# Kernel tuning notes

Hardware: AMD Instinct MI355X
Metric: run time of the kernel (lower is better)

## Reference

```python
import jax, jax.numpy as jnp
import numpy as np

K = 16          # self.nn_size
BALL2 = 0.2     # ball_size * 2, compared against squared L2 dists (faiss convention)

def _knn(q, db, k):
    # squared L2 pairwise distances (B,N,M) via ||q||^2 + ||db||^2 - 2 q.db
    d2 = (jnp.sum(q * q, -1)[..., None]
          + jnp.sum(db * db, -1)[..., None, :]
          - 2.0 * jnp.einsum('bnc,bmc->bnm', q, db))
    neg_d, idx = jax.lax.top_k(-d2, k)   # k smallest distances
    return -neg_d, idx                    # (B,N,K), (B,N,K)

def _cond_numbers(grouped, nball, B, N, C):
    # center by masked-ball mean, then singular values of (K,C) groups
    center = jnp.sum(grouped, axis=2, keepdims=True) / nball[..., None]
    centered = (grouped - center).reshape(-1, K, C)
    S = jnp.linalg.svd(centered, compute_uv=False)   # descending, (B*N, min(K,C))
    return (S[:, 0] / (S[:, -1] + S[:, 0])).reshape(B, N)

def setup_inputs() -> dict:
    key = jax.random.key(0)
    k1, k2 = jax.random.split(key)
    ref_points = jax.random.uniform(k1, (2, 8192, 3), dtype=jnp.float32)
    points = jax.random.uniform(k2, (2, 8192, 3), dtype=jnp.float32)
    return {"ref_points": ref_points, "points": points}

def reference(ref_points, points):
    B, N, C = ref_points.shape
    dist, idx = _knn(ref_points, ref_points, K)
    mask = dist < BALL2                                  # (B,N,K)
    nball = jnp.sum(mask.astype(ref_points.dtype), -1, keepdims=True)  # (B,N,1)

    gather = jax.vmap(lambda p, i: p[i])                 # (N,C),(N,K)->(N,K,C)
    grouped_ref = gather(ref_points, idx)                # (B,N,K,C)
    grouped_ref = jnp.where(mask[..., None], grouped_ref, 0.0)  # masked_fill_ (in-place, kept)
    ref_cond = _cond_numbers(grouped_ref, nball, B, N, C)

    grouped = gather(points, idx)                        # (B,N,K,C)
    # NOTE: original calls masked_fill (non-inplace) and DISCARDS the result -> no masking here
    cond = _cond_numbers(grouped, nball, B, N, C)

    # metric: MSE with mean reduction
    return jnp.mean((cond - ref_cond) ** 2)
```

## Files before the change

### kernel.cpp

```cpp
#include <hip/hip_runtime.h>

#define NPTS   8192
#define KNN    16
#define G      10
#define NCELLS 1000
#define CELLSZ 0.1f
#define BALL2f 0.2f
#define TRUNCM 0xFFFFE000u
#define IDXM   0x1FFFu
#define NBLK   256
#define FLTMAX 3.402823466e+38f

#define WS_ACC    0
#define WS_DONE   8
#define WS_STARTS 16
#define WS_RSORT  8032

__device__ __forceinline__ int clampg(int v) { return v < 0 ? 0 : (v > G - 1 ? G - 1 : v); }

__global__ __launch_bounds__(1024) void prep_kernel(
        const float* __restrict__ ref, int* __restrict__ gstarts,
        float4* __restrict__ rs, double* __restrict__ acc, int* __restrict__ done) {
    __shared__ int cnt[NCELLS];
    __shared__ int ssum[NCELLS + 1];
    __shared__ int wsum[16];
    const int b = blockIdx.x, t = threadIdx.x;
    const int w = t >> 6, lane = t & 63;
    if (b == 0 && t == 0) { acc[0] = 0.0; done[0] = 0; }
    if (t < NCELLS) cnt[t] = 0;
    __syncthreads();

    const float4* rb4 = reinterpret_cast<const float4*>(ref + (size_t)b * NPTS * 3) + t * 6;
    float4 A = rb4[0], B = rb4[1], C = rb4[2], D = rb4[3], E = rb4[4], F = rb4[5];
    float xs[8] = {A.x, A.w, B.z, C.y, D.x, D.w, E.z, F.y};
    float ys[8] = {A.y, B.x, B.w, C.z, D.y, E.x, E.w, F.z};
    float zs[8] = {A.z, B.y, C.x, C.w, D.z, E.y, F.x, F.w};
    int cells[8], slots[8];
    #pragma unroll
    for (int k = 0; k < 8; ++k) {
        int c = (clampg((int)(zs[k] * (float)G)) * G + clampg((int)(ys[k] * (float)G))) * G
              + clampg((int)(xs[k] * (float)G));
        cells[k] = c;
        slots[k] = atomicAdd(&cnt[c], 1);
    }
    __syncthreads();

    int v = (t < NCELLS) ? cnt[t] : 0;
    #pragma unroll
    for (int off = 1; off < 64; off <<= 1) {
        int u = __shfl_up(v, off, 64);
        if (lane >= off) v += u;
    }
    if (lane == 63) wsum[w] = v;
    __syncthreads();
    if (t == 0) {
        int run = 0;
        for (int i2 = 0; i2 < 16; ++i2) { int tv = wsum[i2]; wsum[i2] = run; run += tv; }
    }
    __syncthreads();
    if (t < NCELLS) ssum[t + 1] = v + wsum[w];
    if (t == 0) ssum[0] = 0;
    __syncthreads();
    if (t <= NCELLS) gstarts[b * (NCELLS + 1) + t] = ssum[t];

    #pragma unroll
    for (int k = 0; k < 8; ++k) {
        int pos = ssum[cells[k]] + slots[k];
        rs[(size_t)b * NPTS + pos] = make_float4(xs[k], ys[k], zs[k],
                                                 __uint_as_float((unsigned)(t * 8 + k)));
    }
}

__device__ __noinline__ double cond3(double xx, double xy, double xz,
                                     double yy, double yz, double zz) {
    double q  = (xx + yy + zz) * (1.0 / 3.0);
    double a  = xx - q, b = yy - q, c = zz - q;
    double p1 = xy * xy + xz * xz + yz * yz;
    double p2 = a * a + b * b + c * c + 2.0 * p1;
    if (p2 <= 0.0) return 0.5;
    double p   = sqrt(p2 * (1.0 / 6.0));
    double inv = 1.0 / p;
    double b00 = a * inv, b11 = b * inv, b22 = c * inv;
    double b01 = xy * inv, b02 = xz * inv, b12 = yz * inv;
    double detB = b00 * (b11 * b22 - b12 * b12)
                - b01 * (b01 * b22 - b12 * b02)
                + b02 * (b01 * b12 - b11 * b02);
    double r = 0.5 * detB;
    r = fmin(1.0, fmax(-1.0, r));
    double phi = acos(r) * (1.0 / 3.0);
    double l0 = q + 2.0 * p * cos(phi);
    double l2 = q + 2.0 * p * cos(phi + 2.0943951023931953);
    double s0 = sqrt(fmax(l0, 0.0));
    double s2 = sqrt(fmax(l2, 0.0));
    return s0 / (s0 + s2);
}

__global__ __launch_bounds__(256) void cond_knn_kernel(
        const float* __restrict__ ref, const float* __restrict__ pts,
        const float4* __restrict__ rs, const int* __restrict__ gstarts,
        double* __restrict__ acc, int* __restrict__ done,
        float* __restrict__ out) {
    __shared__ float4 sdb[NPTS];
    __shared__ int ss[NCELLS + 1];
    __shared__ unsigned sld[2][64][17];
    __shared__ unsigned cutp[64];
    __shared__ unsigned char doneA[64];
    __shared__ int flagS;

    const int tid  = threadIdx.x;
    const int w    = tid >> 6;
    const int lane = tid & 63;
    const int b     = blockIdx.x >> 7;
    const int qbase = (blockIdx.x & 127) << 6;
    const float4* rs4 = rs + (size_t)b * NPTS;

    for (int i = tid; i < NPTS; i += 256) sdb[i] = rs4[i];
    for (int i = tid; i < NCELLS + 1; i += 256) ss[i] = gstarts[b * (NCELLS + 1) + i];
    __syncthreads();

    float4 Q = sdb[qbase + lane];
    const float qx = Q.x, qy = Q.y, qz = Q.z;
    const int cx = clampg((int)(qx * (float)G));
    const int cy = clampg((int)(qy * (float)G));
    const int cz = clampg((int)(qz * (float)G));

    unsigned bq[KNN];
    #pragma unroll
    for (int k = 0; k < KNN; ++k) bq[k] = 0xFFFFFFFFu;

    auto ins1 = [&](unsigned vk, unsigned cutv) {
        unsigned cv = cutv < bq[15] ? cutv : bq[15];
        if (vk < cv) {
            bq[15] = vk;
            #pragma unroll
            for (int kk = 15; kk >= 1; --kk) {
                unsigned l2 = min(bq[kk - 1], bq[kk]);
                unsigned h2 = max(bq[kk - 1], bq[kk]);
                bq[kk - 1] = l2; bq[kk] = h2;
            }
        }
    };

    auto scanRange = [&](int s0, int s1, unsigned cutv) {
        int t2 = s0;
        for (; t2 + 4 <= s1; t2 += 4) {
            float4 P0 = sdb[t2 + 0];
            float4 P1 = sdb[t2 + 1];
            float4 P2 = sdb[t2 + 2];
            float4 P3 = sdb[t2 + 3];
            float dx0 = qx - P0.x, dy0 = qy - P0.y, dz0 = qz - P0.z;
            float dx1 = qx - P1.x, dy1 = qy - P1.y, dz1 = qz - P1.z;
            float dx2 = qx - P2.x, dy2 = qy - P2.y, dz2 = qz - P2.z;
            float dx3 = qx - P3.x, dy3 = qy - P3.y, dz3 = qz - P3.z;
            float d0 = fmaf(dx0, dx0, fmaf(dy0, dy0, dz0 * dz0));
            float d1 = fmaf(dx1, dx1, fmaf(dy1, dy1, dz1 * dz1));
            float d2 = fmaf(dx2, dx2, fmaf(dy2, dy2, dz2 * dz2));
            float d3 = fmaf(dx3, dx3, fmaf(dy3, dy3, dz3 * dz3));
            unsigned k0 = (__float_as_uint(d0) & TRUNCM) | __float_as_uint(P0.w);
            unsigned k1 = (__float_as_uint(d1) & TRUNCM) | __float_as_uint(P1.w);
            unsigned k2 = (__float_as_uint(d2) & TRUNCM) | __float_as_uint(P2.w);
            unsigned k3 = (__float_as_uint(d3) & TRUNCM) | __float_as_uint(P3.w);
            unsigned mn = min(min(k0, k1), min(k2, k3));
            unsigned cv = cutv < bq[15] ? cutv : bq[15];
            if (mn < cv) {
                ins1(k0, cutv); ins1(k1, cutv); ins1(k2, cutv); ins1(k3, cutv);
            }
        }
        for (; t2 < s1; ++t2) {
            float4 P = sdb[t2];
            float dx = qx - P.x, dy = qy - P.y, dz = qz - P.z;
            float d = fmaf(dx, dx, fmaf(dy, dy, dz * dz));
            ins1((__float_as_uint(d) & TRUNCM) | __float_as_uint(P.w), cutv);
        }
    };

    for (int it = w; it < 36; it += 4) {
        int q   = it & 3;
        int row = it >> 2;
        int dz = row / 3 - 1;
        int dy = row % 3 - 1;
        int ny = cy + dy, nz = cz + dz;
        if ((unsigned)ny > (unsigned)(G - 1) || (unsigned)nz > (unsigned)(G - 1)) continue;
        int x0 = cx - 1 < 0 ? 0 : cx - 1;
        int x1 = cx + 1 > G - 1 ? G - 1 : cx + 1;
        int c0 = (nz * G + ny) * G + x0;
        int s0 = ss[c0];
        int s1 = ss[c0 + (x1 - x0) + 1];
        int len = s1 - s0;
        int qs = s0 + ((len * q) >> 2);
        int qe = s0 + ((len * (q + 1)) >> 2);
        scanRange(qs, qe, 0xFFFFFFFFu);
    }

    for (int r = 2;; ++r) {
        #pragma unroll
        for (int rnd = 0; rnd < 2; ++rnd) {
            int s = 1 << rnd;
            int slot = w >> (rnd + 1);
            __syncthreads();
            if ((w & (2 * s - 1)) == s) {
                #pragma unroll
                for (int k = 0; k < KNN; ++k) sld[slot][lane][k] = bq[k];
            }
            __syncthreads();
            if ((w & (2 * s - 1)) == 0) {
                unsigned t[KNN];
                #pragma unroll
                for (int i = 0; i < KNN; ++i) t[i] = min(bq[i], sld[slot][lane][KNN - 1 - i]);
                #pragma unroll
                for (int s2 = 8; s2 >= 1; s2 >>= 1) {
                    #pragma unroll
                    for (int i = 0; i < KNN; ++i) {
                        if ((i & s2) == 0) {
                            unsigned l2 = min(t[i], t[i | s2]);
                            unsigned h2 = max(t[i], t[i | s2]);
                            t[i] = l2; t[i | s2] = h2;
                        }
                    }
                }
                #pragma unroll
                for (int k = 0; k < KNN; ++k) bq[k] = t[k];
            }
        }

        if (tid == 0) flagS = 0;
        __syncthreads();
        if (w == 0) {
            int rd = r - 1;
            float mx = FLTMAX;
            if (cx - rd > 0)     mx = fminf(mx, qx - (float)(cx - rd) * CELLSZ);
            if (cx + rd < G - 1) mx = fminf(mx, (float)(cx + rd + 1) * CELLSZ - qx);
            if (cy - rd > 0)     mx = fminf(mx, qy - (float)(cy - rd) * CELLSZ);
            if (cy + rd < G - 1) mx = fminf(mx, (float)(cy + rd + 1) * CELLSZ - qy);
            if (cz - rd > 0)     mx = fminf(mx, qz - (float)(cz - rd) * CELLSZ);
            if (cz + rd < G - 1) mx = fminf(mx, (float)(cz + rd + 1) * CELLSZ - qz);
            float d16t = __uint_as_float(bq[15] & TRUNCM);
            bool dn = d16t <= mx * mx * 0.998f;
            cutp[lane]  = bq[15];
            doneA[lane] = dn ? 1 : 0;
            if (__any(!dn) && lane == 0) flagS = 1;
        }
        __syncthreads();
        if (!flagS || r > G) break;

        if (w != 0) {
            #pragma unroll
            for (int k = 0; k < KNN; ++k) bq[k] = 0xFFFFFFFFu;
        }
        unsigned cut = cutp[lane];
        float cutub = __uint_as_float(cut | IDXM);
        bool active = !doneA[lane];
        int cc = 0;
        for (int dz = -r; dz <= r; ++dz)
        for (int dy = -r; dy <= r; ++dy)
        for (int dx = -r; dx <= r; ++dx) {
            int adx = dx < 0 ? -dx : dx, ady = dy < 0 ? -dy : dy, adz = dz < 0 ? -dz : dz;
            int m = adx > ady ? adx : ady; m = m > adz ? m : adz;
            if (m != r) continue;
            int myc = cc++;
            if ((myc & 3) != w) continue;
            if (!active) continue;
            int nx = cx + dx, ny = cy + dy, nz = cz + dz;
            if ((unsigned)nx > (unsigned)(G - 1) || (unsigned)ny > (unsigned)(G - 1) ||
                (unsigned)nz > (unsigned)(G - 1)) continue;
            float ex0 = (float)nx * CELLSZ;
            float ey0 = (float)ny * CELLSZ;
            float ez0 = (float)nz * CELLSZ;
            float ddx = fmaxf(0.f, fmaxf(ex0 - qx, qx - ex0 - CELLSZ));
            float ddy = fmaxf(0.f, fmaxf(ey0 - qy, qy - ey0 - CELLSZ));
            float ddz = fmaxf(0.f, fmaxf(ez0 - qz, qz - ez0 - CELLSZ));
            float d2min = fmaf(ddx, ddx, fmaf(ddy, ddy, ddz * ddz));
            if (d2min > cutub) continue;
            int cell = (nz * G + ny) * G + nx;
            scanRange(ss[cell], ss[cell + 1], cut);
        }
    }

    if (w != 0) return;

    const float* refb = ref + (size_t)b * NPTS * 3;
    const float* ptsb = pts + (size_t)b * NPTS * 3;
    float rx[KNN], ry[KNN], rz[KNN], px[KNN], py[KNN], pz[KNN];
    int mbits = 0;
    float sRx = 0.f, sRy = 0.f, sRz = 0.f, sPx = 0.f, sPy = 0.f, sPz = 0.f;
    #pragma unroll
    for (int k = 0; k < KNN; ++k) {
        int i = (int)(bq[k] & IDXM);
        float du = __uint_as_float(bq[k] & TRUNCM);
        rx[k] = refb[3 * i]; ry[k] = refb[3 * i + 1]; rz[k] = refb[3 * i + 2];
        px[k] = ptsb[3 * i]; py[k] = ptsb[3 * i + 1]; pz[k] = ptsb[3 * i + 2];
        if (du < BALL2f) {
            mbits |= (1 << k);
            sRx += rx[k]; sRy += ry[k]; sRz += rz[k];
        }
        sPx += px[k]; sPy += py[k]; sPz += pz[k];
    }
    int nb = __popc(mbits);
    double inb = 1.0 / (double)nb;
    double cRx = (double)sRx * inb, cRy = (double)sRy * inb, cRz = (double)sRz * inb;
    double cPx = (double)sPx * inb, cPy = (double)sPy * inb, cPz = (double)sPz * inb;

    double Rxx = 0, Rxy = 0, Rxz = 0, Ryy = 0, Ryz = 0, Rzz = 0;
    double Pxx = 0, Pxy = 0, Pxz = 0, Pyy = 0, Pyz = 0, Pzz = 0;
    #pragma unroll
    for (int k = 0; k < KNN; ++k) {
        bool m = (mbits >> k) & 1;
        double ax = (m ? (double)rx[k] : 0.0) - cRx;
        double ay = (m ? (double)ry[k] : 0.0) - cRy;
        double az = (m ? (double)rz[k] : 0.0) - cRz;
        Rxx += ax * ax; Rxy += ax * ay; Rxz += ax * az;
        Ryy += ay * ay; Ryz += ay * az; Rzz += az * az;
        double bx = (double)px[k] - cPx;
        double by = (double)py[k] - cPy;
        double bz = (double)pz[k] - cPz;
        Pxx += bx * bx; Pxy += bx * by; Pxz += bx * bz;
        Pyy += by * by; Pyz += by * bz; Pzz += bz * bz;
    }
    double condR = cond3(Rxx, Rxy, Rxz, Ryy, Ryz, Rzz);
    double condP = cond3(Pxx, Pxy, Pxz, Pyy, Pyz, Pzz);
    double t = condP - condR;
    t = t * t;

    #pragma unroll
    for (int off = 32; off > 0; off >>= 1) t += __shfl_down(t, off);
    if (lane == 0) {
        atomicAdd(acc, t);
        __threadfence();
        int prev = atomicAdd(done, 1);
        if (prev == NBLK - 1) {
            __threadfence();
            double total = atomicAdd(acc, 0.0);
            out[0] = (float)(total * (1.0 / 16384.0));
        }
    }
}

extern "C" void kernel_launch(void* const* d_in, const int* in_sizes, int n_in,
                              void* d_out, int out_size, void* d_ws, size_t ws_size,
                              hipStream_t stream) {
    const float* ref = (const float*)d_in[0];
    const float* pts = (const float*)d_in[1];
    char* ws = (char*)d_ws;
    double* acc   = (double*)(ws + WS_ACC);
    int* done     = (int*)(ws + WS_DONE);
    int* gstarts  = (int*)(ws + WS_STARTS);
    float4* rsort = (float4*)(ws + WS_RSORT);

    hipLaunchKernelGGL(prep_kernel,     dim3(2),    dim3(1024), 0, stream,
                       ref, gstarts, rsort, acc, done);
    hipLaunchKernelGGL(cond_knn_kernel, dim3(NBLK), dim3(256),  0, stream,
                       ref, pts, rsort, gstarts, acc, done, (float*)d_out);
}
```

Measured before the change: 100.7 us.

## Split each query block's cell scan across 16 waves with tree merge

Raises the kNN block from 4 to 16 wavefronts. Each query's 3x3x3 neighbourhood is now split into 72 chunks, and ring cells are spread over 16 waves. The per-wave top-16 lists are then reduced to wave 0 through a multi-level shared-memory merge tree. This spreads the candidate scan over more waves, since the grid has only 256 blocks. The cost is extra barriers and merge work on every ring iteration, plus more registers per block.

```diff
diff --git a/kernel.cpp b/kernel.cpp
--- a/kernel.cpp
+++ b/kernel.cpp
@@ -95,14 +95,14 @@
     return s0 / (s0 + s2);
 }
 
-__global__ __launch_bounds__(256) void cond_knn_kernel(
+__global__ __launch_bounds__(1024, 4) void cond_knn_kernel(
         const float* __restrict__ ref, const float* __restrict__ pts,
         const float4* __restrict__ rs, const int* __restrict__ gstarts,
         double* __restrict__ acc, int* __restrict__ done,
         float* __restrict__ out) {
     __shared__ float4 sdb[NPTS];
     __shared__ int ss[NCELLS + 1];
-    __shared__ unsigned sld[2][64][17];
+    __shared__ unsigned sld[4][64][17];
     __shared__ unsigned cutp[64];
     __shared__ unsigned char doneA[64];
     __shared__ int flagS;
@@ -114,8 +114,8 @@
     const int qbase = (blockIdx.x & 127) << 6;
     const float4* rs4 = rs + (size_t)b * NPTS;
 
-    for (int i = tid; i < NPTS; i += 256) sdb[i] = rs4[i];
-    for (int i = tid; i < NCELLS + 1; i += 256) ss[i] = gstarts[b * (NCELLS + 1) + i];
+    for (int i = tid; i < NPTS; i += 1024) sdb[i] = rs4[i];
+    for (int i = tid; i < NCELLS + 1; i += 1024) ss[i] = gstarts[b * (NCELLS + 1) + i];
     __syncthreads();
 
     float4 Q = sdb[qbase + lane];
@@ -174,9 +174,54 @@
         }
     };
 
-    for (int it = w; it < 36; it += 4) {
-        int q   = it & 3;
-        int row = it >> 2;
+    auto publish = [&](int slot) {
+        #pragma unroll
+        for (int k = 0; k < KNN; ++k) sld[slot][lane][k] = bq[k];
+    };
+    auto mergeOne = [&](int slot) {
+        unsigned t[KNN];
+        #pragma unroll
+        for (int i = 0; i < KNN; ++i) t[i] = min(bq[i], sld[slot][lane][KNN - 1 - i]);
+        #pragma unroll
+        for (int s2 = 8; s2 >= 1; s2 >>= 1) {
+            #pragma unroll
+            for (int i = 0; i < KNN; ++i) {
+                if ((i & s2) == 0) {
+                    unsigned l2 = min(t[i], t[i | s2]);
+                    unsigned h2 = max(t[i], t[i | s2]);
+                    t[i] = l2; t[i | s2] = h2;
+                }
+            }
+        }
+        #pragma unroll
+        for (int k = 0; k < KNN; ++k) bq[k] = t[k];
+    };
+    auto mergeToW0 = [&]() {
+        __syncthreads();
+        if ((w & 3) == 1) publish(w >> 2);
+        __syncthreads();
+        if ((w & 3) == 0) mergeOne(w >> 2);
+        __syncthreads();
+        if ((w & 3) == 3) publish(w >> 2);
+        __syncthreads();
+        if ((w & 3) == 2) mergeOne(w >> 2);
+        __syncthreads();
+        if ((w & 3) == 2) publish(w >> 2);
+        __syncthreads();
+        if ((w & 3) == 0) mergeOne(w >> 2);
+        __syncthreads();
+        if ((w & 7) == 4) publish(w >> 3);
+        __syncthreads();
+        if ((w & 7) == 0) mergeOne(w >> 3);
+        __syncthreads();
+        if (w == 8) publish(0);
+        __syncthreads();
+        if (w == 0) mergeOne(0);
+    };
+
+    for (int it = w; it < 72; it += 16) {
+        int q   = it & 7;
+        int row = it >> 3;
         int dz = row / 3 - 1;
         int dy = row % 3 - 1;
         int ny = cy + dy, nz = cz + dz;
@@ -187,41 +232,13 @@
         int s0 = ss[c0];
         int s1 = ss[c0 + (x1 - x0) + 1];
         int len = s1 - s0;
-        int qs = s0 + ((len * q) >> 2);
-        int qe = s0 + ((len * (q + 1)) >> 2);
+        int qs = s0 + ((len * q) >> 3);
+        int qe = s0 + ((len * (q + 1)) >> 3);
         scanRange(qs, qe, 0xFFFFFFFFu);
     }
 
     for (int r = 2;; ++r) {
-        #pragma unroll
-        for (int rnd = 0; rnd < 2; ++rnd) {
-            int s = 1 << rnd;
-            int slot = w >> (rnd + 1);
-            __syncthreads();
-            if ((w & (2 * s - 1)) == s) {
-                #pragma unroll
-                for (int k = 0; k < KNN; ++k) sld[slot][lane][k] = bq[k];
-            }
-            __syncthreads();
-            if ((w & (2 * s - 1)) == 0) {
-                unsigned t[KNN];
-                #pragma unroll
-                for (int i = 0; i < KNN; ++i) t[i] = min(bq[i], sld[slot][lane][KNN - 1 - i]);
-                #pragma unroll
-                for (int s2 = 8; s2 >= 1; s2 >>= 1) {
-                    #pragma unroll
-                    for (int i = 0; i < KNN; ++i) {
-                        if ((i & s2) == 0) {
-                            unsigned l2 = min(t[i], t[i | s2]);
-                            unsigned h2 = max(t[i], t[i | s2]);
-                            t[i] = l2; t[i | s2] = h2;
-                        }
-                    }
-                }
-                #pragma unroll
-                for (int k = 0; k < KNN; ++k) bq[k] = t[k];
-            }
-        }
+        mergeToW0();
 
         if (tid == 0) flagS = 0;
         __syncthreads();
@@ -258,7 +275,7 @@
             int m = adx > ady ? adx : ady; m = m > adz ? m : adz;
             if (m != r) continue;
             int myc = cc++;
-            if ((myc & 3) != w) continue;
+            if ((myc & 15) != w) continue;
             if (!active) continue;
             int nx = cx + dx, ny = cy + dy, nz = cz + dz;
             if ((unsigned)nx > (unsigned)(G - 1) || (unsigned)ny > (unsigned)(G - 1) ||
@@ -348,6 +365,6 @@
 
     hipLaunchKernelGGL(prep_kernel,     dim3(2),    dim3(1024), 0, stream,
                        ref, gstarts, rsort, acc, done);
-    hipLaunchKernelGGL(cond_knn_kernel, dim3(NBLK), dim3(256),  0, stream,
+    hipLaunchKernelGGL(cond_knn_kernel, dim3(NBLK), dim3(1024), 0, stream,
                        ref, pts, rsort, gstarts, acc, done, (float*)d_out);
 }
```

New measurement: 100.1 us. No clear change (-0.6%).
